# Optimization experiments

Measured on AMD Instinct MI355X. Metric: run time of the kernel, lower is better.

## Reference

```python
import jax, jax.numpy as jnp
import numpy as np

B, N, D, C, K = 16, 1024, 64, 64, 20
EPS = 1e-3  # keras BatchNormalization default epsilon


def _bn(x, g, b, mu, v):
    return (x - mu) * jax.lax.rsqrt(v + EPS) * g + b


def setup_inputs() -> dict:
    key = jax.random.key(0)
    ks = jax.random.split(key, 6)
    return {
        "feats": jax.random.normal(ks[0], (B, N, D), dtype=jnp.float32),
        "adj": jax.random.uniform(ks[1], (B, N, N), dtype=jnp.float32),
        "w1": jax.random.normal(ks[2], (2 * D, C), dtype=jnp.float32) * 0.05,
        "b1": jax.random.normal(ks[3], (C,), dtype=jnp.float32) * 0.05,
        "g1": jnp.ones((C,), jnp.float32),
        "be1": jnp.zeros((C,), jnp.float32),
        "mu1": jnp.zeros((C,), jnp.float32),
        "v1": jnp.ones((C,), jnp.float32),
        "w2": jax.random.normal(ks[4], (C, C), dtype=jnp.float32) * 0.05,
        "b2": jax.random.normal(ks[5], (C,), dtype=jnp.float32) * 0.05,
        "g2": jnp.ones((C,), jnp.float32),
        "be2": jnp.zeros((C,), jnp.float32),
        "mu2": jnp.zeros((C,), jnp.float32),
        "v2": jnp.ones((C,), jnp.float32),
        "k": K,
    }


def reference(feats, adj, w1, b1, g1, be1, mu1, v1, w2, b2, g2, be2, mu2, v2, k):
    # weighted distance matrix from feature channel 0
    f0 = feats[:, :, 0]                                   # (B,N)
    fdiff = jnp.abs(f0[:, None, :] - f0[:, :, None])       # |f[j]-f[i]| at (b,i,j)
    a = adj * fdiff                                        # (B,N,N)
    # KNN: top_k of negated distance
    _, nn_idx = jax.lax.top_k(-a, k)                       # (B,N,k)
    # edge feature gather
    knn_fts = jax.vmap(lambda f, idx: f[idx])(feats, nn_idx)          # (B,N,k,D)
    center = jnp.broadcast_to(feats[:, :, None, :], knn_fts.shape)    # (B,N,k,D)
    edge = jnp.concatenate([center, knn_fts - center], axis=-1)       # (B,N,k,2D)
    # two fused 1x1 conv + BN + ReLU
    x = jax.nn.relu(_bn(jnp.einsum('bnkd,dc->bnkc', edge, w1) + b1, g1, be1, mu1, v1))
    x = jax.nn.relu(_bn(jnp.einsum('bnkc,ce->bnke', x, w2) + b2, g2, be2, mu2, v2))
    # mean over neighbors
    return jnp.mean(x, axis=2)                             # (B,N,C)
```

## Files before the change

kernel.cpp:

```cpp
#include <hip/hip_runtime.h>
#include <float.h>
#include <math.h>

#define NN 1024
#define DD 64
#define CC 64
#define KK 20
#define EPSL 1e-3f

typedef __attribute__((ext_vector_type(8))) short short8;
typedef __attribute__((ext_vector_type(4))) float f32x4;

__device__ __forceinline__ unsigned short f2bf(float f) {
    unsigned u = __float_as_uint(f);
    return (unsigned short)((u + 0x7fffu + ((u >> 16) & 1u)) >> 16);
}
__device__ __forceinline__ float bf2f(unsigned short h) {
    return __uint_as_float((unsigned)h << 16);
}

__global__ __launch_bounds__(256) void k0_prep(
        const float* __restrict__ w1, const float* __restrict__ w2,
        const float* __restrict__ feats, const float* __restrict__ b1,
        const float* __restrict__ g1, const float* __restrict__ be1,
        const float* __restrict__ mu1, const float* __restrict__ v1,
        unsigned short* __restrict__ b1t, unsigned short* __restrict__ w2t,
        float* __restrict__ bb, float* __restrict__ f0c) {
    int t = blockIdx.x * 256 + threadIdx.x;
    if (t < 8192) {
        int n = t >> 6, k = t & 63;
        float val;
        if (n < 64) {
            float s = g1[n] * rsqrtf(v1[n] + EPSL);
            val = (w1[k * CC + n] - w1[(k + DD) * CC + n]) * s;
        } else {
            int c = n - 64;
            float s = g1[c] * rsqrtf(v1[c] + EPSL);
            val = w1[(k + DD) * CC + c] * s;
        }
        b1t[t] = f2bf(val);
    } else if (t < 12288) {
        int i = t - 8192;
        int n = i >> 6, k = i & 63;
        w2t[i] = f2bf(w2[k * CC + n]);
    } else if (t < 12352) {
        int c = t - 12288;
        float s = g1[c] * rsqrtf(v1[c] + EPSL);
        bb[c] = b1[c] * s + be1[c] - mu1[c] * s;
    } else if (t < 28736) {
        int u = t - 12352;
        f0c[u] = feats[(size_t)u * DD];
    }
}

__global__ __launch_bounds__(256) void k1_mfma(
        const float* __restrict__ feats, const unsigned short* __restrict__ b1t,
        const float* __restrict__ bb,
        unsigned short* __restrict__ cterm, unsigned short* __restrict__ nterm) {
    int lane = threadIdx.x & 63, w = threadIdx.x >> 6;
    int col = lane & 15, quad = lane >> 4;
    int m0 = blockIdx.x * 16;
    int nb = w * 32;

    short8 bfr[2][2];
#pragma unroll
    for (int nt = 0; nt < 2; ++nt)
#pragma unroll
        for (int ks = 0; ks < 2; ++ks)
            bfr[nt][ks] = *(const short8*)(b1t + (nb + nt * 16 + col) * 64 + ks * 32 + quad * 8);

    float bbv[2] = {0.f, 0.f};
    if (w < 2) {
        bbv[0] = bb[nb + col];
        bbv[1] = bb[nb + 16 + col];
    }

    f32x4 acc[2];
    acc[0] = (f32x4)(0.f);
    acc[1] = (f32x4)(0.f);

    const float* fr = feats + (size_t)(m0 + col) * DD;
#pragma unroll
    for (int ks = 0; ks < 2; ++ks) {
        float4 p0 = *(const float4*)(fr + ks * 32 + quad * 8);
        float4 p1 = *(const float4*)(fr + ks * 32 + quad * 8 + 4);
        float f[8] = {p0.x, p0.y, p0.z, p0.w, p1.x, p1.y, p1.z, p1.w};
        short8 ah, al;
#pragma unroll
        for (int i = 0; i < 8; ++i) {
            unsigned short h = f2bf(f[i]);
            ah[i] = (short)h;
            al[i] = (short)f2bf(f[i] - bf2f(h));
        }
#pragma unroll
        for (int nt = 0; nt < 2; ++nt) {
            acc[nt] = __builtin_amdgcn_mfma_f32_16x16x32_bf16(ah, bfr[nt][ks], acc[nt], 0, 0, 0);
            acc[nt] = __builtin_amdgcn_mfma_f32_16x16x32_bf16(al, bfr[nt][ks], acc[nt], 0, 0, 0);
        }
    }

#pragma unroll
    for (int nt = 0; nt < 2; ++nt) {
        int n = nb + nt * 16 + col;
#pragma unroll
        for (int r = 0; r < 4; ++r) {
            int m = m0 + quad * 4 + r;
            unsigned short v = f2bf(acc[nt][r] + bbv[nt]);
            if (w < 2) cterm[(size_t)m * CC + n] = v;
            else       nterm[(size_t)m * CC + (n - 64)] = v;
        }
    }
}

__global__ __launch_bounds__(256) void k2_topk(const float* __restrict__ adj,
                                               const float* __restrict__ f0c,
                                               int* __restrict__ nnidx) {
    __shared__ unsigned long long keybuf[4][64];
    int lane = threadIdx.x & 63;
    int w    = threadIdx.x >> 6;
    int row  = blockIdx.x * 4 + w;
    int b    = row >> 10;
    const float4* arow = (const float4*)(adj + (size_t)row * NN);
    const float4* frow = (const float4*)(f0c + (size_t)b * NN);
    float f0i = f0c[row];
    unsigned vu[16];
#pragma unroll
    for (int tv = 0; tv < 4; ++tv) {
        float4 av = arow[64 * tv + lane];
        float4 fv = frow[64 * tv + lane];
        vu[tv * 4 + 0] = __float_as_uint(av.x * fabsf(fv.x - f0i));
        vu[tv * 4 + 1] = __float_as_uint(av.y * fabsf(fv.y - f0i));
        vu[tv * 4 + 2] = __float_as_uint(av.z * fabsf(fv.z - f0i));
        vu[tv * 4 + 3] = __float_as_uint(av.w * fabsf(fv.w - f0i));
    }
    unsigned x = vu[0];
#pragma unroll
    for (int t = 1; t < 16; ++t) x = (vu[t] < x) ? vu[t] : x;
#pragma unroll
    for (int k = 2; k <= 64; k <<= 1) {
#pragma unroll
        for (int j = k >> 1; j > 0; j >>= 1) {
            unsigned o = __shfl_xor(x, j);
            bool keepmin = (((lane & j) == 0) == ((lane & k) == 0));
            unsigned mn = (o < x) ? o : x;
            unsigned mx = (o < x) ? x : o;
            x = keepmin ? mn : mx;
        }
    }
    unsigned T = __shfl(x, 19);
    int cnt = 0;
#pragma unroll
    for (int t = 0; t < 16; ++t) cnt += (vu[t] <= T) ? 1 : 0;
    int inc = cnt;
#pragma unroll
    for (int off = 1; off < 64; off <<= 1) {
        int o = __shfl_up(inc, off);
        if (lane >= off) inc += o;
    }
    int total = __shfl(inc, 63);
    int* outp = nnidx + (size_t)row * KK;

    if (total <= 64) {
        int pos = inc - cnt;
#pragma unroll
        for (int t = 0; t < 16; ++t) {
            if (vu[t] <= T) {
                int j = 256 * (t >> 2) + 4 * lane + (t & 3);
                keybuf[w][pos] = ((unsigned long long)vu[t] << 32) | (unsigned)j;
                pos++;
            }
        }
        unsigned long long key = (lane < total) ? keybuf[w][lane] : ~0ull;
        unsigned y = (unsigned)(key >> 32);
#pragma unroll
        for (int k = 2; k <= 64; k <<= 1) {
#pragma unroll
            for (int j = k >> 1; j > 0; j >>= 1) {
                unsigned o = __shfl_xor(y, j);
                bool keepmin = (((lane & j) == 0) == ((lane & k) == 0));
                unsigned mn = (o < y) ? o : y;
                unsigned mx = (o < y) ? y : o;
                y = keepmin ? mn : mx;
            }
        }
        unsigned Tstar = __shfl(y, 19);
        bool fl = (lane < total) && ((unsigned)(key >> 32) <= Tstar);
        unsigned long long msk = __ballot(fl);
        int p = __popcll(msk & ((1ull << lane) - 1ull));
        if (fl && p < KK) outp[p] = (int)(unsigned)key;
    } else {
        for (int r = 0; r < KK; ++r) {
            unsigned bv = vu[0];
            int bt = 0;
#pragma unroll
            for (int t = 1; t < 16; ++t) {
                if (vu[t] < bv) { bv = vu[t]; bt = t; }
            }
            int bj = 256 * (bt >> 2) + 4 * lane + (bt & 3);
            unsigned wv = bv;
            int wi = bj;
#pragma unroll
            for (int m = 1; m < 64; m <<= 1) {
                unsigned ov = __shfl_xor(wv, m);
                int oi = __shfl_xor(wi, m);
                if (ov < wv || (ov == wv && oi < wi)) { wv = ov; wi = oi; }
            }
            if (lane == 0) outp[r] = wi;
            if (((wi >> 2) & 63) == lane) {
                int s = ((wi >> 8) << 2) | (wi & 3);
#pragma unroll
                for (int t = 0; t < 16; ++t) {
                    if (t == s) vu[t] = 0xFFFFFFFFu;
                }
            }
        }
    }
}

__global__ __launch_bounds__(256, 3) void k3_mfma(
        const unsigned short* __restrict__ cterm, const unsigned short* __restrict__ nterm,
        const int* __restrict__ nnidx, const unsigned short* __restrict__ w2t,
        const float* __restrict__ b2,
        const float* __restrict__ g2, const float* __restrict__ be2,
        const float* __restrict__ mu2, const float* __restrict__ v2,
        float* __restrict__ out) {
    int lane = threadIdx.x & 63, w = threadIdx.x >> 6;
    int col = lane & 15, quad = lane >> 4;
    int wid = blockIdx.x * 4 + w;
    int u0 = wid * 4;
    int b  = u0 >> 10;

    short8 bfr[4][2];
#pragma unroll
    for (int nt = 0; nt < 4; ++nt)
#pragma unroll
        for (int ks = 0; ks < 2; ++ks)
            bfr[nt][ks] = *(const short8*)(w2t + (nt * 16 + col) * 64 + ks * 32 + quad * 8);

    float s2v[4], sh2v[4];
#pragma unroll
    for (int nt = 0; nt < 4; ++nt) {
        int c = nt * 16 + col;
        float s2 = g2[c] * rsqrtf(v2[c] + EPSL);
        s2v[nt]  = s2;
        sh2v[nt] = (b2[c] - mu2[c]) * s2 + be2[c];
    }

    f32x4 acc[5][4];
#pragma unroll
    for (int mt = 0; mt < 5; ++mt)
#pragma unroll
        for (int nt = 0; nt < 4; ++nt) acc[mt][nt] = (f32x4)(0.f);

    const int* ibase = nnidx + (size_t)u0 * KK;
    int jrow[5];
#pragma unroll
    for (int mt = 0; mt < 5; ++mt) jrow[mt] = ibase[mt * 16 + col];

#pragma unroll
    for (int mt = 0; mt < 5; ++mt) {
        int row = mt * 16 + col;
        int g   = (row * 205) >> 12;
        const unsigned short* np = nterm + (size_t)(b * NN + jrow[mt]) * CC;
        const unsigned short* cp = cterm + (size_t)(u0 + g) * CC;
        short8 afr[2];
#pragma unroll
        for (int ks = 0; ks < 2; ++ks) {
            int ch = ks * 32 + quad * 8;
            short8 nv = *(const short8*)(np + ch);
            short8 cv = *(const short8*)(cp + ch);
#pragma unroll
            for (int i = 0; i < 8; ++i) {
                float h = bf2f((unsigned short)cv[i]) + bf2f((unsigned short)nv[i]);
                afr[ks][i] = (short)f2bf(fmaxf(h, 0.f));
            }
        }
#pragma unroll
        for (int ks = 0; ks < 2; ++ks)
#pragma unroll
            for (int nt = 0; nt < 4; ++nt)
                acc[mt][nt] = __builtin_amdgcn_mfma_f32_16x16x32_bf16(afr[ks], bfr[nt][ks], acc[mt][nt], 0, 0, 0);
    }

    float us0[4] = {0,0,0,0}, us1[4] = {0,0,0,0}, us2[4] = {0,0,0,0}, us3[4] = {0,0,0,0};
#pragma unroll
    for (int mt = 0; mt < 5; ++mt)
#pragma unroll
        for (int nt = 0; nt < 4; ++nt) {
            float qs = 0.f;
#pragma unroll
            for (int r = 0; r < 4; ++r)
                qs += fmaxf(acc[mt][nt][r] * s2v[nt] + sh2v[nt], 0.f);
            if (mt == 0) us0[nt] += qs;
            else if (mt == 4) us3[nt] += qs;
            else if (mt == 1) { float t = (quad >= 1) ? qs : 0.f; us1[nt] += t; us0[nt] += qs - t; }
            else if (mt == 2) { float t = (quad >= 2) ? qs : 0.f; us2[nt] += t; us1[nt] += qs - t; }
            else              { float t = (quad >= 3) ? qs : 0.f; us3[nt] += t; us2[nt] += qs - t; }
        }
#pragma unroll
    for (int nt = 0; nt < 4; ++nt) {
        us0[nt] += __shfl_xor(us0[nt], 16); us0[nt] += __shfl_xor(us0[nt], 32);
        us1[nt] += __shfl_xor(us1[nt], 16); us1[nt] += __shfl_xor(us1[nt], 32);
        us2[nt] += __shfl_xor(us2[nt], 16); us2[nt] += __shfl_xor(us2[nt], 32);
        us3[nt] += __shfl_xor(us3[nt], 16); us3[nt] += __shfl_xor(us3[nt], 32);
    }
#pragma unroll
    for (int nt = 0; nt < 4; ++nt) {
        float v = (quad == 0) ? us0[nt] : (quad == 1) ? us1[nt] : (quad == 2) ? us2[nt] : us3[nt];
        out[(size_t)(u0 + quad) * CC + nt * 16 + col] = v * 0.05f;
    }
}

extern "C" void kernel_launch(void* const* d_in, const int* in_sizes, int n_in,
                              void* d_out, int out_size, void* d_ws, size_t ws_size,
                              hipStream_t stream) {
    const float* feats = (const float*)d_in[0];
    const float* adj   = (const float*)d_in[1];
    const float* w1    = (const float*)d_in[2];
    const float* b1    = (const float*)d_in[3];
    const float* g1    = (const float*)d_in[4];
    const float* be1   = (const float*)d_in[5];
    const float* mu1   = (const float*)d_in[6];
    const float* v1    = (const float*)d_in[7];
    const float* w2    = (const float*)d_in[8];
    const float* b2    = (const float*)d_in[9];
    const float* g2    = (const float*)d_in[10];
    const float* be2   = (const float*)d_in[11];
    const float* mu2   = (const float*)d_in[12];
    const float* v2    = (const float*)d_in[13];
    float* out = (float*)d_out;

    char* ws = (char*)d_ws;
    unsigned short* cterm = (unsigned short*)(ws);
    unsigned short* nterm = (unsigned short*)(ws + 2u * 1024 * 1024);
    float*          f0c   = (float*)(ws + 4u * 1024 * 1024);
    int*            nnidx = (int*)  (ws + 4u * 1024 * 1024 + 64u * 1024);
    unsigned short* b1t   = (unsigned short*)(ws + 6u * 1024 * 1024);
    unsigned short* w2t   = (unsigned short*)(ws + 6u * 1024 * 1024 + 16u * 1024);
    float*          bb    = (float*)(ws + 6u * 1024 * 1024 + 24u * 1024);

    k0_prep<<<113, 256, 0, stream>>>(w1, w2, feats, b1, g1, be1, mu1, v1,
                                     b1t, w2t, bb, f0c);
    k1_mfma<<<1024, 256, 0, stream>>>(feats, b1t, bb, cterm, nterm);
    k2_topk<<<4096, 256, 0, stream>>>(adj, f0c, nnidx);
    k3_mfma<<<1024, 256, 0, stream>>>(cterm, nterm, nnidx, w2t, b2,
                                      g2, be2, mu2, v2, out);
}
```

Baseline: 148.1 us.

## Fuse weight prep into top-k kernel, drop f0 copy, use packed bf16 conversions

Merges the weight/bias preparation kernel into the top-k kernel, which now reads feature channel 0 straight from feats with strided loads instead of from a compacted f0c buffer. This removes one launch and one buffer write. k1 now builds its hi/lo bf16 split by truncation and packs it with bit ops. k3's gather add+ReLU works on packed 32-bit words, truncating to bf16 instead of rounding. The strided feats loads in top-k are uncoalesced and may cost bandwidth, and truncation changes numerics slightly.

```diff
diff --git a/kernel.cpp b/kernel.cpp
--- a/kernel.cpp
+++ b/kernel.cpp
@@ -15,17 +15,15 @@
     unsigned u = __float_as_uint(f);
     return (unsigned short)((u + 0x7fffu + ((u >> 16) & 1u)) >> 16);
 }
-__device__ __forceinline__ float bf2f(unsigned short h) {
-    return __uint_as_float((unsigned)h << 16);
-}
-
-__global__ __launch_bounds__(256) void k0_prep(
+
+__global__ __launch_bounds__(256) void k2_topk_prep(
+        const float* __restrict__ adj, const float* __restrict__ feats,
         const float* __restrict__ w1, const float* __restrict__ w2,
-        const float* __restrict__ feats, const float* __restrict__ b1,
-        const float* __restrict__ g1, const float* __restrict__ be1,
-        const float* __restrict__ mu1, const float* __restrict__ v1,
+        const float* __restrict__ b1, const float* __restrict__ g1,
+        const float* __restrict__ be1, const float* __restrict__ mu1,
+        const float* __restrict__ v1,
         unsigned short* __restrict__ b1t, unsigned short* __restrict__ w2t,
-        float* __restrict__ bb, float* __restrict__ f0c) {
+        float* __restrict__ bb, int* __restrict__ nnidx) {
     int t = blockIdx.x * 256 + threadIdx.x;
     if (t < 8192) {
         int n = t >> 6, k = t & 63;
@@ -47,95 +45,33 @@
         int c = t - 12288;
         float s = g1[c] * rsqrtf(v1[c] + EPSL);
         bb[c] = b1[c] * s + be1[c] - mu1[c] * s;
-    } else if (t < 28736) {
-        int u = t - 12352;
-        f0c[u] = feats[(size_t)u * DD];
-    }
-}
-
-__global__ __launch_bounds__(256) void k1_mfma(
-        const float* __restrict__ feats, const unsigned short* __restrict__ b1t,
-        const float* __restrict__ bb,
-        unsigned short* __restrict__ cterm, unsigned short* __restrict__ nterm) {
-    int lane = threadIdx.x & 63, w = threadIdx.x >> 6;
-    int col = lane & 15, quad = lane >> 4;
-    int m0 = blockIdx.x * 16;
-    int nb = w * 32;
-
-    short8 bfr[2][2];
-#pragma unroll
-    for (int nt = 0; nt < 2; ++nt)
-#pragma unroll
-        for (int ks = 0; ks < 2; ++ks)
-            bfr[nt][ks] = *(const short8*)(b1t + (nb + nt * 16 + col) * 64 + ks * 32 + quad * 8);
-
-    float bbv[2] = {0.f, 0.f};
-    if (w < 2) {
-        bbv[0] = bb[nb + col];
-        bbv[1] = bb[nb + 16 + col];
-    }
-
-    f32x4 acc[2];
-    acc[0] = (f32x4)(0.f);
-    acc[1] = (f32x4)(0.f);
-
-    const float* fr = feats + (size_t)(m0 + col) * DD;
-#pragma unroll
-    for (int ks = 0; ks < 2; ++ks) {
-        float4 p0 = *(const float4*)(fr + ks * 32 + quad * 8);
-        float4 p1 = *(const float4*)(fr + ks * 32 + quad * 8 + 4);
-        float f[8] = {p0.x, p0.y, p0.z, p0.w, p1.x, p1.y, p1.z, p1.w};
-        short8 ah, al;
-#pragma unroll
-        for (int i = 0; i < 8; ++i) {
-            unsigned short h = f2bf(f[i]);
-            ah[i] = (short)h;
-            al[i] = (short)f2bf(f[i] - bf2f(h));
-        }
-#pragma unroll
-        for (int nt = 0; nt < 2; ++nt) {
-            acc[nt] = __builtin_amdgcn_mfma_f32_16x16x32_bf16(ah, bfr[nt][ks], acc[nt], 0, 0, 0);
-            acc[nt] = __builtin_amdgcn_mfma_f32_16x16x32_bf16(al, bfr[nt][ks], acc[nt], 0, 0, 0);
-        }
-    }
-
-#pragma unroll
-    for (int nt = 0; nt < 2; ++nt) {
-        int n = nb + nt * 16 + col;
-#pragma unroll
-        for (int r = 0; r < 4; ++r) {
-            int m = m0 + quad * 4 + r;
-            unsigned short v = f2bf(acc[nt][r] + bbv[nt]);
-            if (w < 2) cterm[(size_t)m * CC + n] = v;
-            else       nterm[(size_t)m * CC + (n - 64)] = v;
-        }
-    }
-}
-
-__global__ __launch_bounds__(256) void k2_topk(const float* __restrict__ adj,
-                                               const float* __restrict__ f0c,
-                                               int* __restrict__ nnidx) {
-    __shared__ unsigned long long keybuf[4][64];
+    }
+
     int lane = threadIdx.x & 63;
     int w    = threadIdx.x >> 6;
     int row  = blockIdx.x * 4 + w;
     int b    = row >> 10;
+    __shared__ unsigned long long keybuf[4][64];
     const float4* arow = (const float4*)(adj + (size_t)row * NN);
-    const float4* frow = (const float4*)(f0c + (size_t)b * NN);
-    float f0i = f0c[row];
+    const float*  fB   = feats + (size_t)b * NN * DD;
+    float f0i = feats[(size_t)row * DD];
     unsigned vu[16];
 #pragma unroll
     for (int tv = 0; tv < 4; ++tv) {
         float4 av = arow[64 * tv + lane];
-        float4 fv = frow[64 * tv + lane];
-        vu[tv * 4 + 0] = __float_as_uint(av.x * fabsf(fv.x - f0i));
-        vu[tv * 4 + 1] = __float_as_uint(av.y * fabsf(fv.y - f0i));
-        vu[tv * 4 + 2] = __float_as_uint(av.z * fabsf(fv.z - f0i));
-        vu[tv * 4 + 3] = __float_as_uint(av.w * fabsf(fv.w - f0i));
+        int j0 = 256 * tv + 4 * lane;
+        float fx = fB[(size_t)(j0 + 0) * DD];
+        float fy = fB[(size_t)(j0 + 1) * DD];
+        float fz = fB[(size_t)(j0 + 2) * DD];
+        float fw = fB[(size_t)(j0 + 3) * DD];
+        vu[tv * 4 + 0] = __float_as_uint(av.x * fabsf(fx - f0i));
+        vu[tv * 4 + 1] = __float_as_uint(av.y * fabsf(fy - f0i));
+        vu[tv * 4 + 2] = __float_as_uint(av.z * fabsf(fz - f0i));
+        vu[tv * 4 + 3] = __float_as_uint(av.w * fabsf(fw - f0i));
     }
     unsigned x = vu[0];
 #pragma unroll
-    for (int t = 1; t < 16; ++t) x = (vu[t] < x) ? vu[t] : x;
+    for (int tt = 1; tt < 16; ++tt) x = (vu[tt] < x) ? vu[tt] : x;
 #pragma unroll
     for (int k = 2; k <= 64; k <<= 1) {
 #pragma unroll
@@ -150,7 +86,7 @@
     unsigned T = __shfl(x, 19);
     int cnt = 0;
 #pragma unroll
-    for (int t = 0; t < 16; ++t) cnt += (vu[t] <= T) ? 1 : 0;
+    for (int tt = 0; tt < 16; ++tt) cnt += (vu[tt] <= T) ? 1 : 0;
     int inc = cnt;
 #pragma unroll
     for (int off = 1; off < 64; off <<= 1) {
@@ -163,10 +99,10 @@
     if (total <= 64) {
         int pos = inc - cnt;
 #pragma unroll
-        for (int t = 0; t < 16; ++t) {
-            if (vu[t] <= T) {
-                int j = 256 * (t >> 2) + 4 * lane + (t & 3);
-                keybuf[w][pos] = ((unsigned long long)vu[t] << 32) | (unsigned)j;
+        for (int tt = 0; tt < 16; ++tt) {
+            if (vu[tt] <= T) {
+                int j = 256 * (tt >> 2) + 4 * lane + (tt & 3);
+                keybuf[w][pos] = ((unsigned long long)vu[tt] << 32) | (unsigned)j;
                 pos++;
             }
         }
@@ -193,8 +129,8 @@
             unsigned bv = vu[0];
             int bt = 0;
 #pragma unroll
-            for (int t = 1; t < 16; ++t) {
-                if (vu[t] < bv) { bv = vu[t]; bt = t; }
+            for (int tt = 1; tt < 16; ++tt) {
+                if (vu[tt] < bv) { bv = vu[tt]; bt = tt; }
             }
             int bj = 256 * (bt >> 2) + 4 * lane + (bt & 3);
             unsigned wv = bv;
@@ -209,10 +145,78 @@
             if (((wi >> 2) & 63) == lane) {
                 int s = ((wi >> 8) << 2) | (wi & 3);
 #pragma unroll
-                for (int t = 0; t < 16; ++t) {
-                    if (t == s) vu[t] = 0xFFFFFFFFu;
+                for (int tt = 0; tt < 16; ++tt) {
+                    if (tt == s) vu[tt] = 0xFFFFFFFFu;
                 }
             }
+        }
+    }
+}
+
+__global__ __launch_bounds__(256) void k1_mfma(
+        const float* __restrict__ feats, const unsigned short* __restrict__ b1t,
+        const float* __restrict__ bb,
+        unsigned short* __restrict__ cterm, unsigned short* __restrict__ nterm) {
+    int lane = threadIdx.x & 63, w = threadIdx.x >> 6;
+    int col = lane & 15, quad = lane >> 4;
+    int m0 = blockIdx.x * 16;
+    int nb = w * 32;
+
+    short8 bfr[2][2];
+#pragma unroll
+    for (int nt = 0; nt < 2; ++nt)
+#pragma unroll
+        for (int ks = 0; ks < 2; ++ks)
+            bfr[nt][ks] = *(const short8*)(b1t + (nb + nt * 16 + col) * 64 + ks * 32 + quad * 8);
+
+    float bbv[2] = {0.f, 0.f};
+    if (w < 2) {
+        bbv[0] = bb[nb + col];
+        bbv[1] = bb[nb + 16 + col];
+    }
+
+    f32x4 acc[2];
+    acc[0] = (f32x4)(0.f);
+    acc[1] = (f32x4)(0.f);
+
+    const float* fr = feats + (size_t)(m0 + col) * DD;
+#pragma unroll
+    for (int ks = 0; ks < 2; ++ks) {
+        float4 p0 = *(const float4*)(fr + ks * 32 + quad * 8);
+        float4 p1 = *(const float4*)(fr + ks * 32 + quad * 8 + 4);
+        float f[8] = {p0.x, p0.y, p0.z, p0.w, p1.x, p1.y, p1.z, p1.w};
+        uint4 hp, lp;
+        unsigned hw[4], lw[4];
+#pragma unroll
+        for (int d = 0; d < 4; ++d) {
+            float a = f[2 * d], bq = f[2 * d + 1];
+            unsigned ua = __float_as_uint(a), ub = __float_as_uint(bq);
+            unsigned am = ua & 0xffff0000u, bm = ub & 0xffff0000u;
+            float ra = a - __uint_as_float(am);
+            float rb = bq - __uint_as_float(bm);
+            hw[d] = bm | (ua >> 16);
+            lw[d] = (__float_as_uint(rb) & 0xffff0000u) | (__float_as_uint(ra) >> 16);
+        }
+        hp.x = hw[0]; hp.y = hw[1]; hp.z = hw[2]; hp.w = hw[3];
+        lp.x = lw[0]; lp.y = lw[1]; lp.z = lw[2]; lp.w = lw[3];
+        short8 ah = __builtin_bit_cast(short8, hp);
+        short8 al = __builtin_bit_cast(short8, lp);
+#pragma unroll
+        for (int nt = 0; nt < 2; ++nt) {
+            acc[nt] = __builtin_amdgcn_mfma_f32_16x16x32_bf16(ah, bfr[nt][ks], acc[nt], 0, 0, 0);
+            acc[nt] = __builtin_amdgcn_mfma_f32_16x16x32_bf16(al, bfr[nt][ks], acc[nt], 0, 0, 0);
+        }
+    }
+
+#pragma unroll
+    for (int nt = 0; nt < 2; ++nt) {
+        int n = nb + nt * 16 + col;
+#pragma unroll
+        for (int r = 0; r < 4; ++r) {
+            int m = m0 + quad * 4 + r;
+            unsigned short v = f2bf(acc[nt][r] + bbv[nt]);
+            if (w < 2) cterm[(size_t)m * CC + n] = v;
+            else       nterm[(size_t)m * CC + (n - 64)] = v;
         }
     }
 }
@@ -267,13 +271,24 @@
 #pragma unroll
         for (int ks = 0; ks < 2; ++ks) {
             int ch = ks * 32 + quad * 8;
-            short8 nv = *(const short8*)(np + ch);
-            short8 cv = *(const short8*)(cp + ch);
-#pragma unroll
-            for (int i = 0; i < 8; ++i) {
-                float h = bf2f((unsigned short)cv[i]) + bf2f((unsigned short)nv[i]);
-                afr[ks][i] = (short)f2bf(fmaxf(h, 0.f));
-            }
+            uint4 cv = *(const uint4*)(cp + ch);
+            uint4 nv = *(const uint4*)(np + ch);
+            unsigned cw[4] = {cv.x, cv.y, cv.z, cv.w};
+            unsigned nw[4] = {nv.x, nv.y, nv.z, nv.w};
+            uint4 rp;
+            unsigned rw[4];
+#pragma unroll
+            for (int d = 0; d < 4; ++d) {
+                float cl = __uint_as_float(cw[d] << 16);
+                float chh = __uint_as_float(cw[d] & 0xffff0000u);
+                float nl = __uint_as_float(nw[d] << 16);
+                float nhh = __uint_as_float(nw[d] & 0xffff0000u);
+                float sl = fmaxf(cl + nl, 0.f);
+                float sh = fmaxf(chh + nhh, 0.f);
+                rw[d] = (__float_as_uint(sh) & 0xffff0000u) | (__float_as_uint(sl) >> 16);
+            }
+            rp.x = rw[0]; rp.y = rw[1]; rp.z = rw[2]; rp.w = rw[3];
+            afr[ks] = __builtin_bit_cast(short8, rp);
         }
 #pragma unroll
         for (int ks = 0; ks < 2; ++ks)
@@ -333,16 +348,15 @@
     char* ws = (char*)d_ws;
     unsigned short* cterm = (unsigned short*)(ws);
     unsigned short* nterm = (unsigned short*)(ws + 2u * 1024 * 1024);
-    float*          f0c   = (float*)(ws + 4u * 1024 * 1024);
-    int*            nnidx = (int*)  (ws + 4u * 1024 * 1024 + 64u * 1024);
+    int*            nnidx = (int*)  (ws + 4u * 1024 * 1024);
     unsigned short* b1t   = (unsigned short*)(ws + 6u * 1024 * 1024);
     unsigned short* w2t   = (unsigned short*)(ws + 6u * 1024 * 1024 + 16u * 1024);
     float*          bb    = (float*)(ws + 6u * 1024 * 1024 + 24u * 1024);
 
-    k0_prep<<<113, 256, 0, stream>>>(w1, w2, feats, b1, g1, be1, mu1, v1,
-                                     b1t, w2t, bb, f0c);
+    k2_topk_prep<<<4096, 256, 0, stream>>>(adj, feats, w1, w2, b1,
+                                           g1, be1, mu1, v1,
+                                           b1t, w2t, bb, nnidx);
     k1_mfma<<<1024, 256, 0, stream>>>(feats, b1t, bb, cterm, nterm);
-    k2_topk<<<4096, 256, 0, stream>>>(adj, f0c, nnidx);
     k3_mfma<<<1024, 256, 0, stream>>>(cterm, nterm, nnidx, w2t, b2,
                                       g2, be2, mu2, v2, out);
 }
```

Measured after the change: 200.0 us. 35.0% more time.
